# Performance work log

Hardware: AMD Instinct MI355X
Metric: run time of the kernel (lower is better)

Reference implementation:

```python
import jax, jax.numpy as jnp
import numpy as np

B, T, D, H = 4096, 512, 32, 16  # batch, time, input feat, LSTM hidden (hardcoded 16 in source)
OUT = 2


def setup_inputs() -> dict:
    key = jax.random.key(0)
    ks = jax.random.split(key, 6)
    x = jax.random.normal(ks[0], (B, T, D), dtype=jnp.float32)
    # LSTM gate weights, flax convention: input-side no bias, hidden-side has bias.
    # Gates packed as [i, f, g, o] along last dim.
    sx = 1.0 / np.sqrt(D)
    sh = 1.0 / np.sqrt(H)
    Wx = jax.random.normal(ks[1], (D, 4 * H), dtype=jnp.float32) * sx
    Wh = jax.random.normal(ks[2], (H, 4 * H), dtype=jnp.float32) * sh
    bh = jnp.zeros((4 * H,), dtype=jnp.float32)
    Wd = jax.random.normal(ks[3], (H, OUT), dtype=jnp.float32) * sh
    bd = jnp.zeros((OUT,), dtype=jnp.float32)
    return {"x": x, "Wx": Wx, "Wh": Wh, "bh": bh, "Wd": Wd, "bd": bd}


def reference(x, Wx, Wh, bh, Wd, bd):
    b = x.shape[0]
    c0 = jnp.zeros((b, H), dtype=x.dtype)
    h0 = jnp.zeros((b, H), dtype=x.dtype)

    def step(carry, xt):  # xt: (B, D)
        c, h = carry
        z = xt @ Wx + h @ Wh + bh  # (B, 4H)
        i, f, g, o = jnp.split(z, 4, axis=-1)
        i = jax.nn.sigmoid(i)
        f = jax.nn.sigmoid(f)
        g = jnp.tanh(g)
        o = jax.nn.sigmoid(o)
        c_new = f * c + i * g
        h_new = o * jnp.tanh(c_new)
        return (c_new, h_new), None

    (c_fin, h_fin), _ = jax.lax.scan(step, (c0, h0), jnp.swapaxes(x, 0, 1))
    # Source uses carry1[0], which in flax LSTMCell is the CELL state c.
    logits = c_fin @ Wd + bd  # (B, 2)
    return jax.nn.softmax(logits, axis=-1)
```

## Files before the change

kernel.cpp:

```cpp
#include <hip/hip_runtime.h>

#define NB 4096
#define NT 512
#define ND 32
#define NH 16
#define CH 16
#define NCH (NT/CH)

typedef float f32x2 __attribute__((ext_vector_type(2)));
typedef float f32x4 __attribute__((ext_vector_type(4)));
typedef short short8 __attribute__((ext_vector_type(8)));
typedef unsigned int uint4v __attribute__((ext_vector_type(4)));

__device__ __forceinline__ unsigned cvt_pk_bf16(float lo, float hi) {
    unsigned r;
    asm("v_cvt_pk_bf16_f32 %0, %1, %2" : "=v"(r) : "v"(lo), "v"(hi));
    return r;
}
__device__ __forceinline__ void pk_fma(f32x2& acc, f32x2 a, f32x2 b) {
    asm("v_pk_fma_f32 %0, %1, %2, %0" : "+v"(acc) : "v"(a), "v"(b));
}
__device__ __forceinline__ float sigm(float y) {
    return __builtin_amdgcn_rcpf(1.0f + __expf(-y));
}
__device__ __forceinline__ float tanh_fast(float y) {
    return fmaf(-2.0f, __builtin_amdgcn_rcpf(1.0f + __expf(2.0f * y)), 1.0f);
}

__global__ __launch_bounds__(256, 1) void lstm4_kernel(
    const float* __restrict__ x,
    const float* __restrict__ Wx,
    const float* __restrict__ Wh,
    const float* __restrict__ bh,
    const float* __restrict__ Wd,
    const float* __restrict__ bd,
    float* __restrict__ out)
{
    __shared__ float zxb[4][4][CH][NH][4];
    __shared__ float hbuf[4][4][NH];

    const int lane = threadIdx.x & 63;
    const int wv = threadIdx.x >> 6;
    const int u = lane & 15;
    const int p = lane >> 4;
    const int k0 = p * 8;

    const int b0 = (blockIdx.x * 4 + wv) * 4;

    short8 bfrag[4];
    float biasn[4];
#pragma unroll
    for (int n = 0; n < 4; ++n) {
        uint4v w;
#pragma unroll
        for (int q = 0; q < 4; ++q)
            w[q] = cvt_pk_bf16(Wx[(k0 + 2 * q) * 64 + n * 16 + u],
                               Wx[(k0 + 2 * q + 1) * 64 + n * 16 + u]);
        bfrag[n] = __builtin_bit_cast(short8, w);
        biasn[n] = bh[n * 16 + u];
    }

    f32x2 wh_i[8], wh_f[8], wh_g[8], wh_o[8];
#pragma unroll
    for (int j = 0; j < 8; ++j) {
        wh_i[j] = f32x2{Wh[(2 * j) * 64 + u],      Wh[(2 * j + 1) * 64 + u]};
        wh_f[j] = f32x2{Wh[(2 * j) * 64 + 16 + u], Wh[(2 * j + 1) * 64 + 16 + u]};
        wh_g[j] = f32x2{Wh[(2 * j) * 64 + 32 + u], Wh[(2 * j + 1) * 64 + 32 + u]};
        wh_o[j] = f32x2{Wh[(2 * j) * 64 + 48 + u], Wh[(2 * j + 1) * 64 + 48 + u]};
    }

    const float* xb[4];
#pragma unroll
    for (int q = 0; q < 4; ++q)
        xb[q] = x + ((size_t)(b0 + q) * NT + u) * ND + k0;

    f32x4 xa[4][2], xn[4][2];
#pragma unroll
    for (int q = 0; q < 4; ++q) {
        xa[q][0] = *(const f32x4*)(xb[q]);
        xa[q][1] = *(const f32x4*)(xb[q] + 4);
    }

    hbuf[wv][p][u] = 0.0f;
    float c = 0.0f;

    for (int tc = 0; tc < NCH; ++tc) {
        const bool have_next = (tc + 1 < NCH);
        if (have_next) {
#pragma unroll
            for (int q = 0; q < 4; ++q) {
                xn[q][0] = *(const f32x4*)(xb[q] + (tc + 1) * CH * ND);
                xn[q][1] = *(const f32x4*)(xb[q] + (tc + 1) * CH * ND + 4);
            }
        }

#pragma unroll
        for (int q = 0; q < 4; ++q) {
            uint4v ua;
            ua[0] = cvt_pk_bf16(xa[q][0].x, xa[q][0].y);
            ua[1] = cvt_pk_bf16(xa[q][0].z, xa[q][0].w);
            ua[2] = cvt_pk_bf16(xa[q][1].x, xa[q][1].y);
            ua[3] = cvt_pk_bf16(xa[q][1].z, xa[q][1].w);
            short8 afrag = __builtin_bit_cast(short8, ua);
            f32x4 acc[4];
#pragma unroll
            for (int n = 0; n < 4; ++n) {
                acc[n] = f32x4{biasn[n], biasn[n], biasn[n], biasn[n]};
                acc[n] = __builtin_amdgcn_mfma_f32_16x16x32_bf16(afrag, bfrag[n], acc[n], 0, 0, 0);
            }
#pragma unroll
            for (int r = 0; r < 4; ++r) {
                f32x4 v = f32x4{acc[0][r], acc[1][r], acc[2][r], acc[3][r]};
                *(f32x4*)&zxb[wv][q][p * 4 + r][u][0] = v;
            }
        }

#pragma unroll
        for (int s = 0; s < CH; ++s) {
            f32x4 zx = *(const f32x4*)&zxb[wv][p][s][u][0];
            f32x4 h0 = *(const f32x4*)&hbuf[wv][p][0];
            f32x4 h1 = *(const f32x4*)&hbuf[wv][p][4];
            f32x4 h2 = *(const f32x4*)&hbuf[wv][p][8];
            f32x4 h3 = *(const f32x4*)&hbuf[wv][p][12];

            f32x2 zi = f32x2{zx.x, 0.0f}, zf = f32x2{zx.y, 0.0f};
            f32x2 zg = f32x2{zx.z, 0.0f}, zo = f32x2{zx.w, 0.0f};
            f32x2 hp;
#define HSTEP(J, HV, A, B)                                            \
            hp = f32x2{HV.A, HV.B};                                   \
            pk_fma(zi, hp, wh_i[J]); pk_fma(zf, hp, wh_f[J]);         \
            pk_fma(zg, hp, wh_g[J]); pk_fma(zo, hp, wh_o[J]);
            HSTEP(0, h0, x, y) HSTEP(1, h0, z, w)
            HSTEP(2, h1, x, y) HSTEP(3, h1, z, w)
            HSTEP(4, h2, x, y) HSTEP(5, h2, z, w)
            HSTEP(6, h3, x, y) HSTEP(7, h3, z, w)
#undef HSTEP
            float ai = sigm(zi.x + zi.y);
            float af = sigm(zf.x + zf.y);
            float ag = tanh_fast(zg.x + zg.y);
            float ao = sigm(zo.x + zo.y);

            float cn = fmaf(af, c, ai * ag);
            c = cn;
            float h = ao * tanh_fast(cn);
            hbuf[wv][p][u] = h;
        }

#pragma unroll
        for (int q = 0; q < 4; ++q) {
            if (have_next) { xa[q][0] = xn[q][0]; xa[q][1] = xn[q][1]; }
        }
    }

    f32x2 wd = *(const f32x2*)&Wd[u * 2];
    float l0 = c * wd.x;
    float l1 = c * wd.y;
#pragma unroll
    for (int m = 1; m < 16; m <<= 1) {
        l0 += __shfl_xor(l0, m);
        l1 += __shfl_xor(l1, m);
    }
    if (u == 0) {
        l0 += bd[0];
        l1 += bd[1];
        float s0 = sigm(l0 - l1);
        float s1 = sigm(l1 - l0);
        *(f32x2*)&out[(b0 + p) * 2] = f32x2{s0, s1};
    }
}

extern "C" void kernel_launch(void* const* d_in, const int* in_sizes, int n_in,
                              void* d_out, int out_size, void* d_ws, size_t ws_size,
                              hipStream_t stream) {
    const float* x  = (const float*)d_in[0];
    const float* Wx = (const float*)d_in[1];
    const float* Wh = (const float*)d_in[2];
    const float* bh = (const float*)d_in[3];
    const float* Wd = (const float*)d_in[4];
    const float* bd = (const float*)d_in[5];
    float* out = (float*)d_out;

    dim3 grid(NB / 16);
    dim3 block(256);
    hipLaunchKernelGGL(lstm4_kernel, grid, block, 0, stream,
                       x, Wx, Wh, bh, Wd, bd, out);
}
```

Baseline: 133.8 us.

## Interleave two independent batch recurrences per wavefront with 64-thread blocks

Each wavefront now carries eight batch rows as two independent sets of four, and interleaves their recurrent steps so the two dependency chains can hide each other's latency. Blocks shrink to a single wave, giving twice as many blocks. The next chunk's x loads and bf16 conversion are split across the step loop to spread memory latency. This costs more registers, since afr holds eight fragments plus staging buffers, which may reduce occupancy.

```diff
diff --git a/kernel.cpp b/kernel.cpp
--- a/kernel.cpp
+++ b/kernel.cpp
@@ -27,7 +27,7 @@
     return fmaf(-2.0f, __builtin_amdgcn_rcpf(1.0f + __expf(2.0f * y)), 1.0f);
 }
 
-__global__ __launch_bounds__(256, 1) void lstm4_kernel(
+__global__ __launch_bounds__(64, 1) void lstm8_kernel(
     const float* __restrict__ x,
     const float* __restrict__ Wx,
     const float* __restrict__ Wh,
@@ -36,16 +36,14 @@
     const float* __restrict__ bd,
     float* __restrict__ out)
 {
-    __shared__ float zxb[4][4][CH][NH][4];
-    __shared__ float hbuf[4][4][NH];
-
-    const int lane = threadIdx.x & 63;
-    const int wv = threadIdx.x >> 6;
+    __shared__ float zxb[8][CH][NH][4];
+    __shared__ float hbuf[2][4][NH];
+
+    const int lane = threadIdx.x;
     const int u = lane & 15;
     const int p = lane >> 4;
     const int k0 = p * 8;
-
-    const int b0 = (blockIdx.x * 4 + wv) * 4;
+    const int b0 = blockIdx.x * 8;
 
     short8 bfrag[4];
     float biasn[4];
@@ -69,103 +67,148 @@
         wh_o[j] = f32x2{Wh[(2 * j) * 64 + 48 + u], Wh[(2 * j + 1) * 64 + 48 + u]};
     }
 
-    const float* xb[4];
-#pragma unroll
-    for (int q = 0; q < 4; ++q)
-        xb[q] = x + ((size_t)(b0 + q) * NT + u) * ND + k0;
-
-    f32x4 xa[4][2], xn[4][2];
-#pragma unroll
-    for (int q = 0; q < 4; ++q) {
-        xa[q][0] = *(const f32x4*)(xb[q]);
-        xa[q][1] = *(const f32x4*)(xb[q] + 4);
-    }
-
-    hbuf[wv][p][u] = 0.0f;
-    float c = 0.0f;
+    const float* xbase = x + ((size_t)b0 * NT + u) * ND + k0;
+
+    uint4v afr[8];
+#pragma unroll
+    for (int g = 0; g < 2; ++g) {
+        f32x4 t0[4], t1[4];
+#pragma unroll
+        for (int q = 0; q < 4; ++q) {
+            const float* src = xbase + (size_t)(g * 4 + q) * NT * ND;
+            t0[q] = *(const f32x4*)(src);
+            t1[q] = *(const f32x4*)(src + 4);
+        }
+#pragma unroll
+        for (int q = 0; q < 4; ++q) {
+            afr[g * 4 + q][0] = cvt_pk_bf16(t0[q].x, t0[q].y);
+            afr[g * 4 + q][1] = cvt_pk_bf16(t0[q].z, t0[q].w);
+            afr[g * 4 + q][2] = cvt_pk_bf16(t1[q].x, t1[q].y);
+            afr[g * 4 + q][3] = cvt_pk_bf16(t1[q].z, t1[q].w);
+        }
+    }
+
+    hbuf[0][p][u] = 0.0f;
+    hbuf[1][p][u] = 0.0f;
+    float c0 = 0.0f, c1 = 0.0f;
+
+#define STEP(SET, QOFF, CREG)                                                 \
+    {                                                                         \
+        f32x4 zx = *(const f32x4*)&zxb[QOFF + p][s][u][0];                    \
+        const f32x4* hv = (const f32x4*)&hbuf[SET][p][0];                     \
+        f32x4 h0 = hv[0], h1 = hv[1], h2 = hv[2], h3 = hv[3];                 \
+        f32x2 zi = f32x2{zx.x, 0.0f}, zf = f32x2{zx.y, 0.0f};                 \
+        f32x2 zg = f32x2{zx.z, 0.0f}, zo = f32x2{zx.w, 0.0f};                 \
+        f32x2 hp;                                                             \
+        hp = f32x2{h0.x, h0.y};                                               \
+        pk_fma(zi, hp, wh_i[0]); pk_fma(zf, hp, wh_f[0]);                     \
+        pk_fma(zg, hp, wh_g[0]); pk_fma(zo, hp, wh_o[0]);                     \
+        hp = f32x2{h0.z, h0.w};                                               \
+        pk_fma(zi, hp, wh_i[1]); pk_fma(zf, hp, wh_f[1]);                     \
+        pk_fma(zg, hp, wh_g[1]); pk_fma(zo, hp, wh_o[1]);                     \
+        hp = f32x2{h1.x, h1.y};                                               \
+        pk_fma(zi, hp, wh_i[2]); pk_fma(zf, hp, wh_f[2]);                     \
+        pk_fma(zg, hp, wh_g[2]); pk_fma(zo, hp, wh_o[2]);                     \
+        hp = f32x2{h1.z, h1.w};                                               \
+        pk_fma(zi, hp, wh_i[3]); pk_fma(zf, hp, wh_f[3]);                     \
+        pk_fma(zg, hp, wh_g[3]); pk_fma(zo, hp, wh_o[3]);                     \
+        hp = f32x2{h2.x, h2.y};                                               \
+        pk_fma(zi, hp, wh_i[4]); pk_fma(zf, hp, wh_f[4]);                     \
+        pk_fma(zg, hp, wh_g[4]); pk_fma(zo, hp, wh_o[4]);                     \
+        hp = f32x2{h2.z, h2.w};                                               \
+        pk_fma(zi, hp, wh_i[5]); pk_fma(zf, hp, wh_f[5]);                     \
+        pk_fma(zg, hp, wh_g[5]); pk_fma(zo, hp, wh_o[5]);                     \
+        hp = f32x2{h3.x, h3.y};                                               \
+        pk_fma(zi, hp, wh_i[6]); pk_fma(zf, hp, wh_f[6]);                     \
+        pk_fma(zg, hp, wh_g[6]); pk_fma(zo, hp, wh_o[6]);                     \
+        hp = f32x2{h3.z, h3.w};                                               \
+        pk_fma(zi, hp, wh_i[7]); pk_fma(zf, hp, wh_f[7]);                     \
+        pk_fma(zg, hp, wh_g[7]); pk_fma(zo, hp, wh_o[7]);                     \
+        float ai = sigm(zi.x + zi.y);                                         \
+        float afv = sigm(zf.x + zf.y);                                        \
+        float ag = tanh_fast(zg.x + zg.y);                                    \
+        float ao = sigm(zo.x + zo.y);                                         \
+        float cn = fmaf(afv, CREG, ai * ag);                                  \
+        CREG = cn;                                                            \
+        hbuf[SET][p][u] = ao * tanh_fast(cn);                                 \
+    }
 
     for (int tc = 0; tc < NCH; ++tc) {
-        const bool have_next = (tc + 1 < NCH);
-        if (have_next) {
-#pragma unroll
-            for (int q = 0; q < 4; ++q) {
-                xn[q][0] = *(const f32x4*)(xb[q] + (tc + 1) * CH * ND);
-                xn[q][1] = *(const f32x4*)(xb[q] + (tc + 1) * CH * ND + 4);
-            }
-        }
-
-#pragma unroll
-        for (int q = 0; q < 4; ++q) {
-            uint4v ua;
-            ua[0] = cvt_pk_bf16(xa[q][0].x, xa[q][0].y);
-            ua[1] = cvt_pk_bf16(xa[q][0].z, xa[q][0].w);
-            ua[2] = cvt_pk_bf16(xa[q][1].x, xa[q][1].y);
-            ua[3] = cvt_pk_bf16(xa[q][1].z, xa[q][1].w);
-            short8 afrag = __builtin_bit_cast(short8, ua);
+#pragma unroll
+        for (int q = 0; q < 8; ++q) {
+            short8 af = __builtin_bit_cast(short8, afr[q]);
             f32x4 acc[4];
 #pragma unroll
             for (int n = 0; n < 4; ++n) {
                 acc[n] = f32x4{biasn[n], biasn[n], biasn[n], biasn[n]};
-                acc[n] = __builtin_amdgcn_mfma_f32_16x16x32_bf16(afrag, bfrag[n], acc[n], 0, 0, 0);
-            }
-#pragma unroll
-            for (int r = 0; r < 4; ++r) {
-                f32x4 v = f32x4{acc[0][r], acc[1][r], acc[2][r], acc[3][r]};
-                *(f32x4*)&zxb[wv][q][p * 4 + r][u][0] = v;
-            }
-        }
+                acc[n] = __builtin_amdgcn_mfma_f32_16x16x32_bf16(af, bfrag[n], acc[n], 0, 0, 0);
+            }
+#pragma unroll
+            for (int r = 0; r < 4; ++r)
+                *(f32x4*)&zxb[q][p * 4 + r][u][0] =
+                    f32x4{acc[0][r], acc[1][r], acc[2][r], acc[3][r]};
+        }
+
+        const bool have_next = (tc + 1 < NCH);
+        const float* xnext = xbase + (size_t)(tc + 1) * CH * ND;
+        f32x4 t0[4], t1[4];
 
 #pragma unroll
         for (int s = 0; s < CH; ++s) {
-            f32x4 zx = *(const f32x4*)&zxb[wv][p][s][u][0];
-            f32x4 h0 = *(const f32x4*)&hbuf[wv][p][0];
-            f32x4 h1 = *(const f32x4*)&hbuf[wv][p][4];
-            f32x4 h2 = *(const f32x4*)&hbuf[wv][p][8];
-            f32x4 h3 = *(const f32x4*)&hbuf[wv][p][12];
-
-            f32x2 zi = f32x2{zx.x, 0.0f}, zf = f32x2{zx.y, 0.0f};
-            f32x2 zg = f32x2{zx.z, 0.0f}, zo = f32x2{zx.w, 0.0f};
-            f32x2 hp;
-#define HSTEP(J, HV, A, B)                                            \
-            hp = f32x2{HV.A, HV.B};                                   \
-            pk_fma(zi, hp, wh_i[J]); pk_fma(zf, hp, wh_f[J]);         \
-            pk_fma(zg, hp, wh_g[J]); pk_fma(zo, hp, wh_o[J]);
-            HSTEP(0, h0, x, y) HSTEP(1, h0, z, w)
-            HSTEP(2, h1, x, y) HSTEP(3, h1, z, w)
-            HSTEP(4, h2, x, y) HSTEP(5, h2, z, w)
-            HSTEP(6, h3, x, y) HSTEP(7, h3, z, w)
-#undef HSTEP
-            float ai = sigm(zi.x + zi.y);
-            float af = sigm(zf.x + zf.y);
-            float ag = tanh_fast(zg.x + zg.y);
-            float ao = sigm(zo.x + zo.y);
-
-            float cn = fmaf(af, c, ai * ag);
-            c = cn;
-            float h = ao * tanh_fast(cn);
-            hbuf[wv][p][u] = h;
-        }
-
-#pragma unroll
-        for (int q = 0; q < 4; ++q) {
-            if (have_next) { xa[q][0] = xn[q][0]; xa[q][1] = xn[q][1]; }
-        }
-    }
+            if (s == 0 && have_next) {
+#pragma unroll
+                for (int q = 0; q < 4; ++q) {
+                    const float* src = xnext + (size_t)q * NT * ND;
+                    t0[q] = *(const f32x4*)(src);
+                    t1[q] = *(const f32x4*)(src + 4);
+                }
+            }
+            if (s == 8 && have_next) {
+#pragma unroll
+                for (int q = 0; q < 4; ++q) {
+                    afr[q][0] = cvt_pk_bf16(t0[q].x, t0[q].y);
+                    afr[q][1] = cvt_pk_bf16(t0[q].z, t0[q].w);
+                    afr[q][2] = cvt_pk_bf16(t1[q].x, t1[q].y);
+                    afr[q][3] = cvt_pk_bf16(t1[q].z, t1[q].w);
+                }
+#pragma unroll
+                for (int q = 0; q < 4; ++q) {
+                    const float* src = xnext + (size_t)(4 + q) * NT * ND;
+                    t0[q] = *(const f32x4*)(src);
+                    t1[q] = *(const f32x4*)(src + 4);
+                }
+            }
+            if (s == 15 && have_next) {
+#pragma unroll
+                for (int q = 0; q < 4; ++q) {
+                    afr[4 + q][0] = cvt_pk_bf16(t0[q].x, t0[q].y);
+                    afr[4 + q][1] = cvt_pk_bf16(t0[q].z, t0[q].w);
+                    afr[4 + q][2] = cvt_pk_bf16(t1[q].x, t1[q].y);
+                    afr[4 + q][3] = cvt_pk_bf16(t1[q].z, t1[q].w);
+                }
+            }
+
+            STEP(0, 0, c0)
+            STEP(1, 4, c1)
+        }
+    }
+#undef STEP
 
     f32x2 wd = *(const f32x2*)&Wd[u * 2];
-    float l0 = c * wd.x;
-    float l1 = c * wd.y;
+    float l0 = c0 * wd.x, l1 = c0 * wd.y;
+    float m0 = c1 * wd.x, m1 = c1 * wd.y;
 #pragma unroll
     for (int m = 1; m < 16; m <<= 1) {
         l0 += __shfl_xor(l0, m);
         l1 += __shfl_xor(l1, m);
+        m0 += __shfl_xor(m0, m);
+        m1 += __shfl_xor(m1, m);
     }
     if (u == 0) {
-        l0 += bd[0];
-        l1 += bd[1];
-        float s0 = sigm(l0 - l1);
-        float s1 = sigm(l1 - l0);
-        *(f32x2*)&out[(b0 + p) * 2] = f32x2{s0, s1};
+        l0 += bd[0]; l1 += bd[1];
+        m0 += bd[0]; m1 += bd[1];
+        *(f32x2*)&out[(b0 + p) * 2]     = f32x2{sigm(l0 - l1), sigm(l1 - l0)};
+        *(f32x2*)&out[(b0 + 4 + p) * 2] = f32x2{sigm(m0 - m1), sigm(m1 - m0)};
     }
 }
 
@@ -180,8 +223,8 @@
     const float* bd = (const float*)d_in[5];
     float* out = (float*)d_out;
 
-    dim3 grid(NB / 16);
-    dim3 block(256);
-    hipLaunchKernelGGL(lstm4_kernel, grid, block, 0, stream,
+    dim3 grid(NB / 8);
+    dim3 block(64);
+    hipLaunchKernelGGL(lstm8_kernel, grid, block, 0, stream,
                        x, Wx, Wh, bh, Wd, bd, out);
 }
```

After: 238.3 us. 78.2% more time.

## Exchange hidden state via xor lane shuffles and prefold log2e into weights

Applied to the files above, without the earlier changes.

The hidden state no longer goes through LDS each step. Each lane keeps its own h, and the recurrent matvec is built from 15 xor-swizzled lane shuffles, with Wh pre-permuted per lane to match. The -log2e (and -2·log2e for the g gate) scaling is folded into Wx, Wh and the bias, so the gate activations use exp2 directly. The next step's zx is also prefetched from LDS. This removes the LDS store-then-load round trip on the serial recurrence, at the cost of more cross-lane shuffle traffic and the loss of packed FMAs.

```diff
diff --git a/kernel.cpp b/kernel.cpp
--- a/kernel.cpp
+++ b/kernel.cpp
@@ -12,22 +12,18 @@
 typedef short short8 __attribute__((ext_vector_type(8)));
 typedef unsigned int uint4v __attribute__((ext_vector_type(4)));
 
+#define LOG2E 1.4426950408889634f
+
 __device__ __forceinline__ unsigned cvt_pk_bf16(float lo, float hi) {
     unsigned r;
     asm("v_cvt_pk_bf16_f32 %0, %1, %2" : "=v"(r) : "v"(lo), "v"(hi));
     return r;
 }
-__device__ __forceinline__ void pk_fma(f32x2& acc, f32x2 a, f32x2 b) {
-    asm("v_pk_fma_f32 %0, %1, %2, %0" : "+v"(acc) : "v"(a), "v"(b));
-}
 __device__ __forceinline__ float sigm(float y) {
     return __builtin_amdgcn_rcpf(1.0f + __expf(-y));
 }
-__device__ __forceinline__ float tanh_fast(float y) {
-    return fmaf(-2.0f, __builtin_amdgcn_rcpf(1.0f + __expf(2.0f * y)), 1.0f);
-}
 
-__global__ __launch_bounds__(256, 1) void lstm4_kernel(
+__global__ __launch_bounds__(256, 1) void lstm_swz_kernel(
     const float* __restrict__ x,
     const float* __restrict__ Wx,
     const float* __restrict__ Wh,
@@ -37,36 +33,36 @@
     float* __restrict__ out)
 {
     __shared__ float zxb[4][4][CH][NH][4];
-    __shared__ float hbuf[4][4][NH];
 
     const int lane = threadIdx.x & 63;
     const int wv = threadIdx.x >> 6;
     const int u = lane & 15;
     const int p = lane >> 4;
     const int k0 = p * 8;
-
     const int b0 = (blockIdx.x * 4 + wv) * 4;
 
     short8 bfrag[4];
     float biasn[4];
 #pragma unroll
     for (int n = 0; n < 4; ++n) {
+        const float sn = (n == 2) ? (-2.0f * LOG2E) : (-LOG2E);
         uint4v w;
 #pragma unroll
         for (int q = 0; q < 4; ++q)
-            w[q] = cvt_pk_bf16(Wx[(k0 + 2 * q) * 64 + n * 16 + u],
-                               Wx[(k0 + 2 * q + 1) * 64 + n * 16 + u]);
+            w[q] = cvt_pk_bf16(sn * Wx[(k0 + 2 * q) * 64 + n * 16 + u],
+                               sn * Wx[(k0 + 2 * q + 1) * 64 + n * 16 + u]);
         bfrag[n] = __builtin_bit_cast(short8, w);
-        biasn[n] = bh[n * 16 + u];
+        biasn[n] = sn * bh[n * 16 + u];
     }
 
-    f32x2 wh_i[8], wh_f[8], wh_g[8], wh_o[8];
+    float whr_i[16], whr_f[16], whr_g[16], whr_o[16];
 #pragma unroll
-    for (int j = 0; j < 8; ++j) {
-        wh_i[j] = f32x2{Wh[(2 * j) * 64 + u],      Wh[(2 * j + 1) * 64 + u]};
-        wh_f[j] = f32x2{Wh[(2 * j) * 64 + 16 + u], Wh[(2 * j + 1) * 64 + 16 + u]};
-        wh_g[j] = f32x2{Wh[(2 * j) * 64 + 32 + u], Wh[(2 * j + 1) * 64 + 32 + u]};
-        wh_o[j] = f32x2{Wh[(2 * j) * 64 + 48 + u], Wh[(2 * j + 1) * 64 + 48 + u]};
+    for (int m = 0; m < 16; ++m) {
+        const int k = (u ^ m);
+        whr_i[m] = -LOG2E * Wh[k * 64 + u];
+        whr_f[m] = -LOG2E * Wh[k * 64 + 16 + u];
+        whr_g[m] = -2.0f * LOG2E * Wh[k * 64 + 32 + u];
+        whr_o[m] = -LOG2E * Wh[k * 64 + 48 + u];
     }
 
     const float* xb[4];
@@ -81,8 +77,7 @@
         xa[q][1] = *(const f32x4*)(xb[q] + 4);
     }
 
-    hbuf[wv][p][u] = 0.0f;
-    float c = 0.0f;
+    float c = 0.0f, h = 0.0f;
 
     for (int tc = 0; tc < NCH; ++tc) {
         const bool have_next = (tc + 1 < NCH);
@@ -109,41 +104,42 @@
                 acc[n] = __builtin_amdgcn_mfma_f32_16x16x32_bf16(afrag, bfrag[n], acc[n], 0, 0, 0);
             }
 #pragma unroll
-            for (int r = 0; r < 4; ++r) {
-                f32x4 v = f32x4{acc[0][r], acc[1][r], acc[2][r], acc[3][r]};
-                *(f32x4*)&zxb[wv][q][p * 4 + r][u][0] = v;
-            }
+            for (int r = 0; r < 4; ++r)
+                *(f32x4*)&zxb[wv][q][p * 4 + r][u][0] =
+                    f32x4{acc[0][r], acc[1][r], acc[2][r], acc[3][r]};
         }
 
+        f32x4 zx_cur = *(const f32x4*)&zxb[wv][p][0][u][0];
 #pragma unroll
         for (int s = 0; s < CH; ++s) {
-            f32x4 zx = *(const f32x4*)&zxb[wv][p][s][u][0];
-            f32x4 h0 = *(const f32x4*)&hbuf[wv][p][0];
-            f32x4 h1 = *(const f32x4*)&hbuf[wv][p][4];
-            f32x4 h2 = *(const f32x4*)&hbuf[wv][p][8];
-            f32x4 h3 = *(const f32x4*)&hbuf[wv][p][12];
+            f32x4 zx_nxt;
+            if (s + 1 < CH)
+                zx_nxt = *(const f32x4*)&zxb[wv][p][s + 1][u][0];
 
-            f32x2 zi = f32x2{zx.x, 0.0f}, zf = f32x2{zx.y, 0.0f};
-            f32x2 zg = f32x2{zx.z, 0.0f}, zo = f32x2{zx.w, 0.0f};
-            f32x2 hp;
-#define HSTEP(J, HV, A, B)                                            \
-            hp = f32x2{HV.A, HV.B};                                   \
-            pk_fma(zi, hp, wh_i[J]); pk_fma(zf, hp, wh_f[J]);         \
-            pk_fma(zg, hp, wh_g[J]); pk_fma(zo, hp, wh_o[J]);
-            HSTEP(0, h0, x, y) HSTEP(1, h0, z, w)
-            HSTEP(2, h1, x, y) HSTEP(3, h1, z, w)
-            HSTEP(4, h2, x, y) HSTEP(5, h2, z, w)
-            HSTEP(6, h3, x, y) HSTEP(7, h3, z, w)
-#undef HSTEP
-            float ai = sigm(zi.x + zi.y);
-            float af = sigm(zf.x + zf.y);
-            float ag = tanh_fast(zg.x + zg.y);
-            float ao = sigm(zo.x + zo.y);
+            float zi = zx_cur.x + h * whr_i[0];
+            float zf = zx_cur.y + h * whr_f[0];
+            float zg = zx_cur.z + h * whr_g[0];
+            float zo = zx_cur.w + h * whr_o[0];
+#pragma unroll
+            for (int m = 1; m < 16; ++m) {
+                float hm = __shfl_xor(h, m);
+                zi = fmaf(hm, whr_i[m], zi);
+                zf = fmaf(hm, whr_f[m], zf);
+                zg = fmaf(hm, whr_g[m], zg);
+                zo = fmaf(hm, whr_o[m], zo);
+            }
+
+            float ai = __builtin_amdgcn_rcpf(1.0f + exp2f(zi));
+            float af = __builtin_amdgcn_rcpf(1.0f + exp2f(zf));
+            float ag = fmaf(2.0f, __builtin_amdgcn_rcpf(1.0f + exp2f(zg)), -1.0f);
+            float ao = __builtin_amdgcn_rcpf(1.0f + exp2f(zo));
 
             float cn = fmaf(af, c, ai * ag);
             c = cn;
-            float h = ao * tanh_fast(cn);
-            hbuf[wv][p][u] = h;
+            float t = fmaf(2.0f, __builtin_amdgcn_rcpf(
+                               1.0f + exp2f((-2.0f * LOG2E) * cn)), -1.0f);
+            h = ao * t;
+            zx_cur = zx_nxt;
         }
 
 #pragma unroll
@@ -163,9 +159,7 @@
     if (u == 0) {
         l0 += bd[0];
         l1 += bd[1];
-        float s0 = sigm(l0 - l1);
-        float s1 = sigm(l1 - l0);
-        *(f32x2*)&out[(b0 + p) * 2] = f32x2{s0, s1};
+        *(f32x2*)&out[(b0 + p) * 2] = f32x2{sigm(l0 - l1), sigm(l1 - l0)};
     }
 }
 
@@ -182,6 +176,6 @@
 
     dim3 grid(NB / 16);
     dim3 block(256);
-    hipLaunchKernelGGL(lstm4_kernel, grid, block, 0, stream,
+    hipLaunchKernelGGL(lstm_swz_kernel, grid, block, 0, stream,
                        x, Wx, Wh, bh, Wd, bd, out);
 }
```

After: 234.2 us. 1.75x slower.
